# Kernel optimization log

Measured on AMD Instinct MI355X. Metric: run time of the kernel, lower is better.

Reference implementation:

```python
import jax, jax.numpy as jnp
import numpy as np

IN_FEATURES = 1024
NUM_EXPERTS = 64
TOP_K = 2


def setup_inputs() -> dict:
    key = jax.random.key(0)
    kx, kw, kb = jax.random.split(key, 3)
    x = jax.random.normal(kx, (8, 4096, IN_FEATURES), dtype=jnp.float32)
    # nn.Linear init scale ~ 1/sqrt(in_features)
    bound = 1.0 / np.sqrt(IN_FEATURES)
    W = jax.random.uniform(kw, (NUM_EXPERTS, IN_FEATURES), dtype=jnp.float32, minval=-bound, maxval=bound)
    b = jax.random.uniform(kb, (NUM_EXPERTS,), dtype=jnp.float32, minval=-bound, maxval=bound)
    return {"x": x, "W": W, "b": b}


def reference(x, W, b):
    # logits: [B, S, E]
    logits = jnp.einsum("bsd,ed->bse", x, W) + b
    gates = jax.nn.softmax(logits, axis=-1)
    top_k_gates, top_k_indices = jax.lax.top_k(gates, TOP_K)
    return top_k_gates, top_k_indices
```

## Files before the change

### kernel.cpp

```cpp
#include <hip/hip_runtime.h>

#define D 1024
#define E 64
#define TPB 256
#define TOKS 64
#define NCH 8
#define CHB 32768

typedef __attribute__((ext_vector_type(8))) short bf16x8;
typedef __attribute__((ext_vector_type(8))) unsigned short u16x8;
typedef __attribute__((ext_vector_type(4))) float f32x4;
typedef __attribute__((ext_vector_type(4))) unsigned int u32x4;

__device__ __forceinline__ unsigned short bf16_rne(float f) {
    unsigned u = __builtin_bit_cast(unsigned, f);
    u += 0x7fffu + ((u >> 16) & 1u);
    return (unsigned short)(u >> 16);
}
__device__ __forceinline__ float bf16_to_f(unsigned short h) {
    unsigned u = ((unsigned)h) << 16;
    return __builtin_bit_cast(float, u);
}
__device__ __forceinline__ unsigned cvt_pk_bf16(float a, float b) {
    unsigned r;
    asm("v_cvt_pk_bf16_f32 %0, %1, %2" : "=v"(r) : "v"(a), "v"(b));
    return r;
}
__device__ __forceinline__ float lo_val(unsigned p) {
    return __builtin_bit_cast(float, p << 16);
}
__device__ __forceinline__ float hi_val(unsigned p) {
    return __builtin_bit_cast(float, p & 0xffff0000u);
}

__device__ __forceinline__ void gload16(const void* g, void* l) {
    __builtin_amdgcn_global_load_lds(
        (const __attribute__((address_space(1))) unsigned int*)g,
        (__attribute__((address_space(3))) unsigned int*)l, 16, 0, 0);
}

__device__ __forceinline__ void split8_rne(f32x4 a, f32x4 b, bf16x8& hv, bf16x8& lv) {
    unsigned h0 = cvt_pk_bf16(a[0], a[1]);
    unsigned h1 = cvt_pk_bf16(a[2], a[3]);
    unsigned h2 = cvt_pk_bf16(b[0], b[1]);
    unsigned h3 = cvt_pk_bf16(b[2], b[3]);
    unsigned l0 = cvt_pk_bf16(a[0] - lo_val(h0), a[1] - hi_val(h0));
    unsigned l1 = cvt_pk_bf16(a[2] - lo_val(h1), a[3] - hi_val(h1));
    unsigned l2 = cvt_pk_bf16(b[0] - lo_val(h2), b[1] - hi_val(h2));
    unsigned l3 = cvt_pk_bf16(b[2] - lo_val(h3), b[3] - hi_val(h3));
    hv = __builtin_bit_cast(bf16x8, (u32x4){h0, h1, h2, h3});
    lv = __builtin_bit_cast(bf16x8, (u32x4){l0, l1, l2, l3});
}

__global__ __launch_bounds__(256) void router_prep(
        const float* __restrict__ W, unsigned short* __restrict__ Ws) {
    int t = blockIdx.x * 256 + threadIdx.x;
    int lane = t & 63;
    int nt = (t >> 6) & 3;
    int ks = t >> 8;
    int n = lane & 15, q = lane >> 4;
    const float* src = W + (size_t)(nt * 16 + n) * D + ks * 32 + q * 8;
    u16x8 hv, lv;
#pragma unroll
    for (int j = 0; j < 8; ++j) {
        float v = src[j];
        unsigned short h = bf16_rne(v);
        hv[j] = h;
        lv[j] = bf16_rne(v - bf16_to_f(h));
    }
    size_t base = ((size_t)(ks * 8 + nt * 2) * 64 + lane) * 8;
    *(u16x8*)(Ws + base)          = hv;
    *(u16x8*)(Ws + base + 64 * 8) = lv;
}

__global__ __launch_bounds__(TPB) void router_main(
        const float* __restrict__ x, const unsigned short* __restrict__ Ws,
        const float* __restrict__ bias, float* __restrict__ out, int T) {
    __shared__ __align__(16) union SM {
        unsigned char buf[2][CHB];
        float ls[TOKS][E + 1];
    } sm;
    __shared__ float sbias[E];

    const int tid  = threadIdx.x;
    const int lane = tid & 63;
    const int wid  = tid >> 6;
    const int n    = lane & 15;
    const int q    = lane >> 4;
    const int t0   = blockIdx.x * TOKS;

    if (tid < E) sbias[tid] = bias[tid];

    const float* arow = x + (size_t)(t0 + wid * 16 + n) * D + q * 8;
    const u32x4* gws  = (const u32x4*)Ws;

    f32x4 c0 = {0.f, 0.f, 0.f, 0.f}, c1 = c0, c2 = c0, c3 = c0;

    f32x4 A0u, A0v, A1u, A1v, A2u, A2v, A3u, A3v;
    f32x4 N0u, N0v, N1u, N1v, N2u, N2v, N3u, N3v;

#define GLOADW(bi_, c_) do {                                          \
        const u32x4* _g = gws + (size_t)(c_) * 2048 + tid;            \
        char* _lb = (char*)sm.buf[bi_] + wid * 1024;                  \
        gload16(_g,        _lb);                                      \
        gload16(_g + 256,  _lb + 4096);                               \
        gload16(_g + 512,  _lb + 8192);                               \
        gload16(_g + 768,  _lb + 12288);                              \
        gload16(_g + 1024, _lb + 16384);                              \
        gload16(_g + 1280, _lb + 20480);                              \
        gload16(_g + 1536, _lb + 24576);                              \
        gload16(_g + 1792, _lb + 28672);                              \
    } while (0)

#define ISSUEA(p0u,p0v,p1u,p1v,p2u,p2v,p3u,p3v, c_) do {              \
        const float* _b = arow + (size_t)(c_) * 128;                  \
        p0u = *(const f32x4*)(_b);       p0v = *(const f32x4*)(_b + 4);   \
        p1u = *(const f32x4*)(_b + 32);  p1v = *(const f32x4*)(_b + 36);  \
        p2u = *(const f32x4*)(_b + 64);  p2v = *(const f32x4*)(_b + 68);  \
        p3u = *(const f32x4*)(_b + 96);  p3v = *(const f32x4*)(_b + 100); \
    } while (0)

#define MFMA __builtin_amdgcn_mfma_f32_16x16x32_bf16
#define COMPSTEP(bi_, ksl_, au_, av_) do {                            \
        bf16x8 ah, al;                                                \
        split8_rne(au_, av_, ah, al);                                 \
        const char* _p = (const char*)sm.buf[bi_] + (ksl_) * 8192 + lane * 16; \
        {                                                             \
            bf16x8 bh = *(const bf16x8*)(_p);                         \
            bf16x8 bl = *(const bf16x8*)(_p + 1024);                  \
            c0 = MFMA(ah, bh, c0, 0, 0, 0);                           \
            c0 = MFMA(al, bh, c0, 0, 0, 0);                           \
            c0 = MFMA(ah, bl, c0, 0, 0, 0);                           \
        }                                                             \
        {                                                             \
            bf16x8 bh = *(const bf16x8*)(_p + 2048);                  \
            bf16x8 bl = *(const bf16x8*)(_p + 3072);                  \
            c1 = MFMA(ah, bh, c1, 0, 0, 0);                           \
            c1 = MFMA(al, bh, c1, 0, 0, 0);                           \
            c1 = MFMA(ah, bl, c1, 0, 0, 0);                           \
        }                                                             \
        {                                                             \
            bf16x8 bh = *(const bf16x8*)(_p + 4096);                  \
            bf16x8 bl = *(const bf16x8*)(_p + 5120);                  \
            c2 = MFMA(ah, bh, c2, 0, 0, 0);                           \
            c2 = MFMA(al, bh, c2, 0, 0, 0);                           \
            c2 = MFMA(ah, bl, c2, 0, 0, 0);                           \
        }                                                             \
        {                                                             \
            bf16x8 bh = *(const bf16x8*)(_p + 6144);                  \
            bf16x8 bl = *(const bf16x8*)(_p + 7168);                  \
            c3 = MFMA(ah, bh, c3, 0, 0, 0);                           \
            c3 = MFMA(al, bh, c3, 0, 0, 0);                           \
            c3 = MFMA(ah, bl, c3, 0, 0, 0);                           \
        }                                                             \
    } while (0)

#define COMPCHUNK(bi_, p0u,p0v,p1u,p1v,p2u,p2v,p3u,p3v) do {          \
        COMPSTEP(bi_, 0, p0u, p0v);                                   \
        COMPSTEP(bi_, 1, p1u, p1v);                                   \
        COMPSTEP(bi_, 2, p2u, p2v);                                   \
        COMPSTEP(bi_, 3, p3u, p3v);                                   \
    } while (0)

    GLOADW(0, 0);
    ISSUEA(A0u,A0v,A1u,A1v,A2u,A2v,A3u,A3v, 0);
    __syncthreads();

    for (int c = 0; c < NCH; c += 2) {
        GLOADW(1, c + 1);
        ISSUEA(N0u,N0v,N1u,N1v,N2u,N2v,N3u,N3v, c + 1);
        COMPCHUNK(0, A0u,A0v,A1u,A1v,A2u,A2v,A3u,A3v);
        __syncthreads();
        GLOADW(0, (c + 2) & (NCH - 1));
        ISSUEA(A0u,A0v,A1u,A1v,A2u,A2v,A3u,A3v, (c + 2) & (NCH - 1));
        COMPCHUNK(1, N0u,N0v,N1u,N1v,N2u,N2v,N3u,N3v);
        __syncthreads();
    }

    {
        const int row = wid * 16 + q * 4;
#define STORE_C(c_, nt_) do {                                         \
            int col = (nt_) * 16 + n;                                 \
            float bv = sbias[col];                                    \
            sm.ls[row + 0][col] = c_[0] + bv;                         \
            sm.ls[row + 1][col] = c_[1] + bv;                         \
            sm.ls[row + 2][col] = c_[2] + bv;                         \
            sm.ls[row + 3][col] = c_[3] + bv;                         \
        } while (0)
        STORE_C(c0, 0); STORE_C(c1, 1); STORE_C(c2, 2); STORE_C(c3, 3);
#undef STORE_C
    }
    __syncthreads();

    if (tid < TOKS) {
        float m1 = -3.4e38f, m2 = -3.4e38f;
        int i1 = 0, i2 = 0;
        for (int e = 0; e < E; ++e) {
            float v = sm.ls[tid][e];
            if (v > m1) { m2 = m1; i2 = i1; m1 = v; i1 = e; }
            else if (v > m2) { m2 = v; i2 = e; }
        }
        float Z = 0.f;
        for (int e = 0; e < E; ++e) Z += __expf(sm.ls[tid][e] - m1);
        float inv = 1.f / Z;
        int gt = t0 + tid;
        out[(size_t)gt * 2]     = inv;
        out[(size_t)gt * 2 + 1] = __expf(m2 - m1) * inv;
        float* oi = out + (size_t)T * 2;
        oi[(size_t)gt * 2]     = (float)i1;
        oi[(size_t)gt * 2 + 1] = (float)i2;
    }
}

extern "C" void kernel_launch(void* const* d_in, const int* in_sizes, int n_in,
                              void* d_out, int out_size, void* d_ws, size_t ws_size,
                              hipStream_t stream) {
    const float* x = (const float*)d_in[0];
    const float* W = (const float*)d_in[1];
    const float* b = (const float*)d_in[2];
    float* out = (float*)d_out;
    unsigned short* Ws = (unsigned short*)d_ws;
    int T = in_sizes[0] / D;
    hipLaunchKernelGGL(router_prep, dim3(32), dim3(256), 0, stream, W, Ws);
    hipLaunchKernelGGL(router_main, dim3(T / TOKS), dim3(TPB), 0, stream,
                       x, Ws, b, out, T);
}
```

Baseline: 203.7 us.

## Double tokens per block and stage weight matrix in two LDS halves

Each block now handles 128 tokens instead of 64, and each wave computes two 16-row token tiles against every LDS-resident weight fragment, so each B fragment read from LDS is reused twice. The double-buffered per-chunk weight pipeline is replaced by loading half of the split-bf16 weight matrix (128KB) into LDS at once, computing over it, then loading the second half. This cuts the number of barriers and halves the weight traffic per token, at the cost of one block per CU (launch_bounds 1), exposed weight-load latency between the halves, and more registers for the doubled accumulators and A prefetch sets.

```diff
diff --git a/kernel.cpp b/kernel.cpp
--- a/kernel.cpp
+++ b/kernel.cpp
@@ -3,9 +3,8 @@
 #define D 1024
 #define E 64
 #define TPB 256
-#define TOKS 64
-#define NCH 8
-#define CHB 32768
+#define TOKS 128
+#define HALFB 131072
 
 typedef __attribute__((ext_vector_type(8))) short bf16x8;
 typedef __attribute__((ext_vector_type(8))) unsigned short u16x8;
@@ -32,7 +31,6 @@
 __device__ __forceinline__ float hi_val(unsigned p) {
     return __builtin_bit_cast(float, p & 0xffff0000u);
 }
-
 __device__ __forceinline__ void gload16(const void* g, void* l) {
     __builtin_amdgcn_global_load_lds(
         (const __attribute__((address_space(1))) unsigned int*)g,
@@ -73,11 +71,14 @@
     *(u16x8*)(Ws + base + 64 * 8) = lv;
 }
 
-__global__ __launch_bounds__(TPB) void router_main(
+struct Aset { f32x4 s0, s1, s2, s3, s4, s5, s6, s7; };
+struct Acc  { f32x4 c0, c1, c2, c3, d0, d1, d2, d3; };
+
+__global__ __launch_bounds__(TPB, 1) void router_main(
         const float* __restrict__ x, const unsigned short* __restrict__ Ws,
         const float* __restrict__ bias, float* __restrict__ out, int T) {
     __shared__ __align__(16) union SM {
-        unsigned char buf[2][CHB];
+        unsigned char w[HALFB];
         float ls[TOKS][E + 1];
     } sm;
     __shared__ float sbias[E];
@@ -91,103 +92,134 @@
 
     if (tid < E) sbias[tid] = bias[tid];
 
-    const float* arow = x + (size_t)(t0 + wid * 16 + n) * D + q * 8;
-    const u32x4* gws  = (const u32x4*)Ws;
-
-    f32x4 c0 = {0.f, 0.f, 0.f, 0.f}, c1 = c0, c2 = c0, c3 = c0;
-
-    f32x4 A0u, A0v, A1u, A1v, A2u, A2v, A3u, A3v;
-    f32x4 N0u, N0v, N1u, N1v, N2u, N2v, N3u, N3v;
-
-#define GLOADW(bi_, c_) do {                                          \
-        const u32x4* _g = gws + (size_t)(c_) * 2048 + tid;            \
-        char* _lb = (char*)sm.buf[bi_] + wid * 1024;                  \
-        gload16(_g,        _lb);                                      \
-        gload16(_g + 256,  _lb + 4096);                               \
-        gload16(_g + 512,  _lb + 8192);                               \
-        gload16(_g + 768,  _lb + 12288);                              \
-        gload16(_g + 1024, _lb + 16384);                              \
-        gload16(_g + 1280, _lb + 20480);                              \
-        gload16(_g + 1536, _lb + 24576);                              \
-        gload16(_g + 1792, _lb + 28672);                              \
-    } while (0)
-
-#define ISSUEA(p0u,p0v,p1u,p1v,p2u,p2v,p3u,p3v, c_) do {              \
-        const float* _b = arow + (size_t)(c_) * 128;                  \
-        p0u = *(const f32x4*)(_b);       p0v = *(const f32x4*)(_b + 4);   \
-        p1u = *(const f32x4*)(_b + 32);  p1v = *(const f32x4*)(_b + 36);  \
-        p2u = *(const f32x4*)(_b + 64);  p2v = *(const f32x4*)(_b + 68);  \
-        p3u = *(const f32x4*)(_b + 96);  p3v = *(const f32x4*)(_b + 100); \
+    const float* ar0 = x + (size_t)(t0 + wid * 32 + n) * D + q * 8;
+    const float* ar1 = ar0 + (size_t)16 * D;
+    const u32x4* gws = (const u32x4*)Ws;
+    const char* ldsp = (const char*)sm.w + lane * 16;
+
+    Acc acc;
+    acc.c0 = (f32x4){0.f,0.f,0.f,0.f}; acc.c1 = acc.c0; acc.c2 = acc.c0; acc.c3 = acc.c0;
+    acc.d0 = acc.c0; acc.d1 = acc.c0; acc.d2 = acc.c0; acc.d3 = acc.c0;
+
+#define GLOADHALF(h_) do {                                            \
+        const u32x4* _g = gws + (size_t)(h_) * 8192 + tid;            \
+        char* _lb = (char*)sm.w + wid * 1024;                         \
+        _Pragma("unroll")                                             \
+        for (int r = 0; r < 32; ++r)                                  \
+            gload16(_g + r * 256, _lb + r * 4096);                    \
     } while (0)
 
 #define MFMA __builtin_amdgcn_mfma_f32_16x16x32_bf16
-#define COMPSTEP(bi_, ksl_, au_, av_) do {                            \
-        bf16x8 ah, al;                                                \
+
+#define COMPSTEP(ksl_, au_, av_, bu_, bv_) do {                       \
+        bf16x8 ah, al, eh, el;                                        \
         split8_rne(au_, av_, ah, al);                                 \
-        const char* _p = (const char*)sm.buf[bi_] + (ksl_) * 8192 + lane * 16; \
+        split8_rne(bu_, bv_, eh, el);                                 \
+        const char* _p = ldsp + (ksl_) * 8192;                        \
         {                                                             \
             bf16x8 bh = *(const bf16x8*)(_p);                         \
             bf16x8 bl = *(const bf16x8*)(_p + 1024);                  \
-            c0 = MFMA(ah, bh, c0, 0, 0, 0);                           \
-            c0 = MFMA(al, bh, c0, 0, 0, 0);                           \
-            c0 = MFMA(ah, bl, c0, 0, 0, 0);                           \
+            acc.c0 = MFMA(ah, bh, acc.c0, 0, 0, 0);                   \
+            acc.c0 = MFMA(al, bh, acc.c0, 0, 0, 0);                   \
+            acc.c0 = MFMA(ah, bl, acc.c0, 0, 0, 0);                   \
+            acc.d0 = MFMA(eh, bh, acc.d0, 0, 0, 0);                   \
+            acc.d0 = MFMA(el, bh, acc.d0, 0, 0, 0);                   \
+            acc.d0 = MFMA(eh, bl, acc.d0, 0, 0, 0);                   \
         }                                                             \
         {                                                             \
             bf16x8 bh = *(const bf16x8*)(_p + 2048);                  \
             bf16x8 bl = *(const bf16x8*)(_p + 3072);                  \
-            c1 = MFMA(ah, bh, c1, 0, 0, 0);                           \
-            c1 = MFMA(al, bh, c1, 0, 0, 0);                           \
-            c1 = MFMA(ah, bl, c1, 0, 0, 0);                           \
+            acc.c1 = MFMA(ah, bh, acc.c1, 0, 0, 0);                   \
+            acc.c1 = MFMA(al, bh, acc.c1, 0, 0, 0);                   \
+            acc.c1 = MFMA(ah, bl, acc.c1, 0, 0, 0);                   \
+            acc.d1 = MFMA(eh, bh, acc.d1, 0, 0, 0);                   \
+            acc.d1 = MFMA(el, bh, acc.d1, 0, 0, 0);                   \
+            acc.d1 = MFMA(eh, bl, acc.d1, 0, 0, 0);                   \
         }                                                             \
         {                                                             \
             bf16x8 bh = *(const bf16x8*)(_p + 4096);                  \
             bf16x8 bl = *(const bf16x8*)(_p + 5120);                  \
-            c2 = MFMA(ah, bh, c2, 0, 0, 0);                           \
-            c2 = MFMA(al, bh, c2, 0, 0, 0);                           \
-            c2 = MFMA(ah, bl, c2, 0, 0, 0);                           \
+            acc.c2 = MFMA(ah, bh, acc.c2, 0, 0, 0);                   \
+            acc.c2 = MFMA(al, bh, acc.c2, 0, 0, 0);                   \
+            acc.c2 = MFMA(ah, bl, acc.c2, 0, 0, 0);                   \
+            acc.d2 = MFMA(eh, bh, acc.d2, 0, 0, 0);                   \
+            acc.d2 = MFMA(el, bh, acc.d2, 0, 0, 0);                   \
+            acc.d2 = MFMA(eh, bl, acc.d2, 0, 0, 0);                   \
         }                                                             \
         {                                                             \
             bf16x8 bh = *(const bf16x8*)(_p + 6144);                  \
             bf16x8 bl = *(const bf16x8*)(_p + 7168);                  \
-            c3 = MFMA(ah, bh, c3, 0, 0, 0);                           \
-            c3 = MFMA(al, bh, c3, 0, 0, 0);                           \
-            c3 = MFMA(ah, bl, c3, 0, 0, 0);                           \
-        }                                                             \
-    } while (0)
-
-#define COMPCHUNK(bi_, p0u,p0v,p1u,p1v,p2u,p2v,p3u,p3v) do {          \
-        COMPSTEP(bi_, 0, p0u, p0v);                                   \
-        COMPSTEP(bi_, 1, p1u, p1v);                                   \
-        COMPSTEP(bi_, 2, p2u, p2v);                                   \
-        COMPSTEP(bi_, 3, p3u, p3v);                                   \
-    } while (0)
-
-    GLOADW(0, 0);
-    ISSUEA(A0u,A0v,A1u,A1v,A2u,A2v,A3u,A3v, 0);
-    __syncthreads();
-
-    for (int c = 0; c < NCH; c += 2) {
-        GLOADW(1, c + 1);
-        ISSUEA(N0u,N0v,N1u,N1v,N2u,N2v,N3u,N3v, c + 1);
-        COMPCHUNK(0, A0u,A0v,A1u,A1v,A2u,A2v,A3u,A3v);
-        __syncthreads();
-        GLOADW(0, (c + 2) & (NCH - 1));
-        ISSUEA(A0u,A0v,A1u,A1v,A2u,A2v,A3u,A3v, (c + 2) & (NCH - 1));
-        COMPCHUNK(1, N0u,N0v,N1u,N1v,N2u,N2v,N3u,N3v);
-        __syncthreads();
-    }
+            acc.c3 = MFMA(ah, bh, acc.c3, 0, 0, 0);                   \
+            acc.c3 = MFMA(al, bh, acc.c3, 0, 0, 0);                   \
+            acc.c3 = MFMA(ah, bl, acc.c3, 0, 0, 0);                   \
+            acc.d3 = MFMA(eh, bh, acc.d3, 0, 0, 0);                   \
+            acc.d3 = MFMA(el, bh, acc.d3, 0, 0, 0);                   \
+            acc.d3 = MFMA(eh, bl, acc.d3, 0, 0, 0);                   \
+        }                                                             \
+    } while (0)
+
+#define ISSUEA(S_, ks_) do {                                          \
+        S_.s0 = *(const f32x4*)(ar0 + (ks_) * 32);                    \
+        S_.s1 = *(const f32x4*)(ar0 + (ks_) * 32 + 4);                \
+        S_.s2 = *(const f32x4*)(ar0 + (ks_) * 32 + 32);               \
+        S_.s3 = *(const f32x4*)(ar0 + (ks_) * 32 + 36);               \
+        S_.s4 = *(const f32x4*)(ar1 + (ks_) * 32);                    \
+        S_.s5 = *(const f32x4*)(ar1 + (ks_) * 32 + 4);                \
+        S_.s6 = *(const f32x4*)(ar1 + (ks_) * 32 + 32);               \
+        S_.s7 = *(const f32x4*)(ar1 + (ks_) * 32 + 36);               \
+    } while (0)
+
+#define COMP2(ksl_, S_) do {                                          \
+        COMPSTEP((ksl_),     S_.s0, S_.s1, S_.s4, S_.s5);             \
+        COMPSTEP((ksl_) + 1, S_.s2, S_.s3, S_.s6, S_.s7);             \
+    } while (0)
+
+    Aset P, Q;
+
+    GLOADHALF(0);
+    ISSUEA(P, 0);
+    __syncthreads();
+
+    ISSUEA(Q, 2);  COMP2(0,  P);
+    ISSUEA(P, 4);  COMP2(2,  Q);
+    ISSUEA(Q, 6);  COMP2(4,  P);
+    ISSUEA(P, 8);  COMP2(6,  Q);
+    ISSUEA(Q, 10); COMP2(8,  P);
+    ISSUEA(P, 12); COMP2(10, Q);
+    ISSUEA(Q, 14); COMP2(12, P);
+    ISSUEA(P, 16); COMP2(14, Q);
+
+    __syncthreads();
+    GLOADHALF(1);
+    __syncthreads();
+
+    ISSUEA(Q, 18); COMP2(0,  P);
+    ISSUEA(P, 20); COMP2(2,  Q);
+    ISSUEA(Q, 22); COMP2(4,  P);
+    ISSUEA(P, 24); COMP2(6,  Q);
+    ISSUEA(Q, 26); COMP2(8,  P);
+    ISSUEA(P, 28); COMP2(10, Q);
+    ISSUEA(Q, 30); COMP2(12, P);
+    COMP2(14, Q);
+
+    __syncthreads();
 
     {
-        const int row = wid * 16 + q * 4;
-#define STORE_C(c_, nt_) do {                                         \
+        const int row = wid * 32 + q * 4;
+#define STORE_C(cc_, dd_, nt_) do {                                   \
             int col = (nt_) * 16 + n;                                 \
             float bv = sbias[col];                                    \
-            sm.ls[row + 0][col] = c_[0] + bv;                         \
-            sm.ls[row + 1][col] = c_[1] + bv;                         \
-            sm.ls[row + 2][col] = c_[2] + bv;                         \
-            sm.ls[row + 3][col] = c_[3] + bv;                         \
+            sm.ls[row + 0][col] = cc_[0] + bv;                        \
+            sm.ls[row + 1][col] = cc_[1] + bv;                        \
+            sm.ls[row + 2][col] = cc_[2] + bv;                        \
+            sm.ls[row + 3][col] = cc_[3] + bv;                        \
+            sm.ls[row + 16][col] = dd_[0] + bv;                       \
+            sm.ls[row + 17][col] = dd_[1] + bv;                       \
+            sm.ls[row + 18][col] = dd_[2] + bv;                       \
+            sm.ls[row + 19][col] = dd_[3] + bv;                       \
         } while (0)
-        STORE_C(c0, 0); STORE_C(c1, 1); STORE_C(c2, 2); STORE_C(c3, 3);
+        STORE_C(acc.c0, acc.d0, 0); STORE_C(acc.c1, acc.d1, 1);
+        STORE_C(acc.c2, acc.d2, 2); STORE_C(acc.c3, acc.d3, 3);
 #undef STORE_C
     }
     __syncthreads();
```

Measured after the change: 212.9 us. 4.5% more time.
